# Performance work log

Hardware: AMD Instinct MI355X
Metric: run time of the kernel (lower is better)

## Reference

```python
import jax, jax.numpy as jnp
import numpy as np

EPS = 1e-5
G = 8    # groups
K = 3    # kernel_size


def bn(x, gamma, beta, mean, var):
    # inference-mode BatchNorm2d; x: (b,C,H,W), params: (C,)
    inv = gamma / jnp.sqrt(var + EPS)
    return x * inv[None, :, None, None] + (beta - mean * inv)[None, :, None, None]


def gconv1x1(x, w):
    # grouped 1x1 conv; x: (b, g*ci, H, W), w: (g, co, ci) -> (b, g*co, H, W)
    b, C, H, W = x.shape
    g, co, ci = w.shape
    xg = x.reshape(b, g, ci, H, W)
    y = jnp.einsum('bgihw,goi->bgohw', xg, w)
    return y.reshape(b, g * co, H, W)


def unfold3(x):
    # torch.nn.Unfold(k=3, stride=1, dilation=1, padding=1), reshaped to (b, C, 9, H, W)
    b, C, H, W = x.shape
    xp = jnp.pad(x, ((0, 0), (0, 0), (1, 1), (1, 1)))
    patches = [xp[:, :, i:i + H, j:j + W] for i in range(K) for j in range(K)]
    return jnp.stack(patches, axis=2)


def setup_inputs() -> dict:
    key = jax.random.key(0)
    ks = jax.random.split(key, 16)
    f = jax.random.normal
    u = jax.random.uniform
    return {
        'x':  f(ks[0], (2, 256, 128, 128), jnp.float32),
        'w1': f(ks[1], (8, 8, 32), jnp.float32) * 0.1,
        'b1': f(ks[2], (64,), jnp.float32) * 0.1,
        'g1': u(ks[3], (64,), jnp.float32, 0.5, 1.5),
        'be1': f(ks[4], (64,), jnp.float32) * 0.1,
        'm1': f(ks[5], (64,), jnp.float32) * 0.1,
        'v1': u(ks[6], (64,), jnp.float32, 0.5, 1.5),
        'w2': f(ks[7], (8, 10, 8), jnp.float32) * 0.1,
        'b2': f(ks[8], (80,), jnp.float32) * 0.1,
        'g2': u(ks[9], (80,), jnp.float32, 0.5, 1.5),
        'be2': f(ks[10], (80,), jnp.float32) * 0.1,
        'm2': f(ks[11], (80,), jnp.float32) * 0.1,
        'v2': u(ks[12], (80,), jnp.float32, 0.5, 1.5),
        'wv': f(ks[13], (8, 32, 32), jnp.float32) * 0.1,
    }


def reference(x, w1, b1, g1, be1, m1, v1, w2, b2, g2, be2, m2, v2, wv):
    b, C, H, W = x.shape
    # mask_conv: grouped 1x1 conv -> BN -> tanh -> grouped 1x1 conv -> BN
    t = jnp.tanh(bn(gconv1x1(x, w1) + b1[None, :, None, None], g1, be1, m1, v1))
    mn = bn(gconv1x1(t, w2) + b2[None, :, None, None], g2, be2, m2, v2)  # (b, G*(1+K*K), H, W)
    neighbor = mn[:, :G]          # (b, G, H, W)
    mask = mn[:, G:]              # (b, G*K*K, H, W)
    nb = unfold3(neighbor)        # (b, G, 9, H, W)
    logits = mask.reshape(b, G, K * K, H, W) + nb
    attn = jax.nn.softmax(logits, axis=2)               # (b, G, 9, H, W)
    # value path: grouped 1x1 conv (no bias) then unfold
    v = gconv1x1(x, wv)                                  # (b, C, H, W)
    vu = unfold3(v).reshape(b, G, C // G, K * K, H, W)   # (b, G, C/G, 9, H, W)
    out = jnp.einsum('bgkhw,bgckhw->bgchw', attn, vu)    # weighted sum over window
    return out.reshape(b, C, H, W)
```

## Files before the change

### kernel.cpp

```cpp
#include <hip/hip_runtime.h>

#define HW  16384
#define WD  128

#define TS   16
#define HS   18
#define HP   (HS * HS)
#define PRS  20
#define PLS  360
#define SROW 80

typedef __attribute__((ext_vector_type(8))) short bf16x8;
typedef __attribute__((ext_vector_type(4))) float f32x4;

__device__ __forceinline__ unsigned short f2bf(float f) {
    unsigned int u = __builtin_bit_cast(unsigned int, f);
    u += 0x7FFFu + ((u >> 16) & 1u);
    return (unsigned short)(u >> 16);
}
__device__ __forceinline__ float bf2f(unsigned int s) {
    return __builtin_bit_cast(float, (s & 0xFFFFu) << 16);
}
__device__ __forceinline__ float ftanh(float v) {
    const float e = __expf(2.0f * v);
    return 1.0f - __fdividef(2.0f, e + 1.0f);
}

__global__ __launch_bounds__(256) void la_t(
    const float* __restrict__ x,
    const float* __restrict__ w1, const float* __restrict__ b1,
    const float* __restrict__ g1, const float* __restrict__ be1,
    const float* __restrict__ m1, const float* __restrict__ v1,
    ushort4* __restrict__ t4, uint4* __restrict__ xbf)
{
    const int z   = blockIdx.x;
    const int b   = blockIdx.y;
    const int pix = blockIdx.z * blockDim.x + threadIdx.x;
    const int p   = z & 7;
    const int h   = z >> 3;

    const float* xp = x + (size_t)(b * 256 + p * 32) * HW + pix;
    float xv[32];
#pragma unroll
    for (int c = 0; c < 32; ++c) xv[c] = xp[(size_t)c * HW];

#pragma unroll
    for (int j = 0; j < 2; ++j) {
        const int c8 = h * 2 + j;
        uint4 u;
        u.x = (unsigned)f2bf(xv[c8 * 8 + 0]) | ((unsigned)f2bf(xv[c8 * 8 + 1]) << 16);
        u.y = (unsigned)f2bf(xv[c8 * 8 + 2]) | ((unsigned)f2bf(xv[c8 * 8 + 3]) << 16);
        u.z = (unsigned)f2bf(xv[c8 * 8 + 4]) | ((unsigned)f2bf(xv[c8 * 8 + 5]) << 16);
        u.w = (unsigned)f2bf(xv[c8 * 8 + 6]) | ((unsigned)f2bf(xv[c8 * 8 + 7]) << 16);
        xbf[((size_t)((b * 8 + p) * 4 + c8)) * HW + pix] = u;
    }

    const float* w1g = w1 + p * 256 + h * 4 * 32;
    float tv[4];
#pragma unroll
    for (int o = 0; o < 4; ++o) {
        float a = 0.f;
#pragma unroll
        for (int ci = 0; ci < 32; ++ci) a = fmaf(xv[ci], w1g[o * 32 + ci], a);
        const int ch = p * 8 + h * 4 + o;
        const float inv = g1[ch] * rsqrtf(v1[ch] + 1e-5f);
        const float add = be1[ch] + (b1[ch] - m1[ch]) * inv;
        tv[o] = ftanh(fmaf(a, inv, add));
    }

    t4[((size_t)((b * 8 + p) * 2 + h)) * HW + pix] =
        make_ushort4(f2bf(tv[0]), f2bf(tv[1]), f2bf(tv[2]), f2bf(tv[3]));
}

__global__ __launch_bounds__(256) void la_fused(
    const float* __restrict__ w2, const float* __restrict__ b2,
    const float* __restrict__ g2, const float* __restrict__ be2,
    const float* __restrict__ m2, const float* __restrict__ v2,
    const float* __restrict__ wv,
    const ushort4* __restrict__ t4, const uint4* __restrict__ xbf,
    float* __restrict__ out)
{
    __shared__ uint4 xt[4 * PLS];
    __shared__ float nbs[PLS];

    const int tid  = threadIdx.x;
    const int bg   = blockIdx.x;
    const int tile = blockIdx.y;
    const int b    = bg >> 3, g = bg & 7;
    const int ty0  = (tile >> 3) * TS;
    const int tx0  = (tile & 7) * TS;
    const int lane = tid & 63, wv4 = tid >> 6;

    const uint4*   xg = xbf + (size_t)((b * 8 + g) * 4) * HW;
    const ushort4* t0 = t4  + (size_t)(b * 16) * HW;

    const float* wvg = wv + g * 1024;
    bf16x8 bfrag[2];
#pragma unroll
    for (int nt = 0; nt < 2; ++nt) {
        const float* wp = wvg + (nt * 16 + (lane & 15)) * 32 + (lane >> 4) * 8;
        bf16x8 f;
#pragma unroll
        for (int j = 0; j < 8; ++j) f[j] = (short)f2bf(wp[j]);
        bfrag[nt] = f;
    }

    const int cy  = tid >> 4, cx = tid & 15;
    const int cpx = (ty0 + cy) * WD + (tx0 + cx);

    const int mc0    = 8 + 9 * g;
    const int pa     = mc0 / 10;
    const int pb     = (mc0 + 8) / 10;
    const int ksplit = 10 - (mc0 - pa * 10);

    const ushort4 tAlo = t4[((size_t)((b * 8 + pa) * 2 + 0)) * HW + cpx];
    const ushort4 tAhi = t4[((size_t)((b * 8 + pa) * 2 + 1)) * HW + cpx];
    const ushort4 tBlo = t4[((size_t)((b * 8 + pb) * 2 + 0)) * HW + cpx];
    const ushort4 tBhi = t4[((size_t)((b * 8 + pb) * 2 + 1)) * HW + cpx];

    const float inv2n = g2[g] * rsqrtf(v2[g] + 1e-5f);
    const float add2n = be2[g] + (b2[g] - m2[g]) * inv2n;

    for (int hp = tid; hp < HP; hp += 256) {
        const int hy = hp / HS, hx = hp - hy * HS;
        const int iy = ty0 + hy - 1, ix = tx0 + hx - 1;
        const int slot = hy * PRS + hx;
        if (((unsigned)iy < 128u) && ((unsigned)ix < 128u)) {
            const int po = iy * WD + ix;
            const ushort4 ta = t0[po];
            const ushort4 tb = t0[(size_t)HW + po];
            float an = 0.f;
            an = fmaf(bf2f(ta.x), w2[g * 8 + 0], an);
            an = fmaf(bf2f(ta.y), w2[g * 8 + 1], an);
            an = fmaf(bf2f(ta.z), w2[g * 8 + 2], an);
            an = fmaf(bf2f(ta.w), w2[g * 8 + 3], an);
            an = fmaf(bf2f(tb.x), w2[g * 8 + 4], an);
            an = fmaf(bf2f(tb.y), w2[g * 8 + 5], an);
            an = fmaf(bf2f(tb.z), w2[g * 8 + 6], an);
            an = fmaf(bf2f(tb.w), w2[g * 8 + 7], an);
            nbs[slot] = fmaf(an, inv2n, add2n);
#pragma unroll
            for (int c8 = 0; c8 < 4; ++c8)
                xt[c8 * PLS + slot] = xg[(size_t)c8 * HW + po];
        } else {
            const uint4 z = make_uint4(0u, 0u, 0u, 0u);
#pragma unroll
            for (int c8 = 0; c8 < 4; ++c8) xt[c8 * PLS + slot] = z;
            nbs[slot] = 0.f;
        }
    }
    __syncthreads();

    float tA[8], tB[8];
    tA[0] = bf2f(tAlo.x); tA[1] = bf2f(tAlo.y);
    tA[2] = bf2f(tAlo.z); tA[3] = bf2f(tAlo.w);
    tA[4] = bf2f(tAhi.x); tA[5] = bf2f(tAhi.y);
    tA[6] = bf2f(tAhi.z); tA[7] = bf2f(tAhi.w);
    tB[0] = bf2f(tBlo.x); tB[1] = bf2f(tBlo.y);
    tB[2] = bf2f(tBlo.z); tB[3] = bf2f(tBlo.w);
    tB[4] = bf2f(tBhi.x); tB[5] = bf2f(tBhi.y);
    tB[6] = bf2f(tBhi.z); tB[7] = bf2f(tBhi.w);

    float lg[9];
    float mx = -1e30f;
#pragma unroll
    for (int k = 0; k < 9; ++k) {
        const int mc = mc0 + k;
        const int p  = (k < ksplit) ? pa : pb;
        const int o  = mc - p * 10;
        const float* w2p = w2 + p * 80 + o * 8;
        float a = 0.f;
#pragma unroll
        for (int i = 0; i < 8; ++i) {
            const float ti = (k < ksplit) ? tA[i] : tB[i];
            a = fmaf(ti, w2p[i], a);
        }
        const float inv = g2[mc] * rsqrtf(v2[mc] + 1e-5f);
        const float add = be2[mc] + (b2[mc] - m2[mc]) * inv;
        lg[k] = fmaf(a, inv, add) + nbs[(cy + k / 3) * PRS + (cx + k % 3)];
        mx = fmaxf(mx, lg[k]);
    }
    float ssum = 0.f;
#pragma unroll
    for (int k = 0; k < 9; ++k) { lg[k] = __expf(lg[k] - mx); ssum += lg[k]; }
    const float rs = 1.f / ssum;

    float s[32];
#pragma unroll
    for (int c = 0; c < 32; ++c) s[c] = 0.f;
#pragma unroll
    for (int k = 0; k < 9; ++k) {
        const int slot = (cy + k / 3) * PRS + (cx + k % 3);
        const float e = lg[k];
#pragma unroll
        for (int c8 = 0; c8 < 4; ++c8) {
            const uint4 u = xt[c8 * PLS + slot];
            s[c8 * 8 + 0] = fmaf(e, bf2f(u.x),       s[c8 * 8 + 0]);
            s[c8 * 8 + 1] = fmaf(e, bf2f(u.x >> 16), s[c8 * 8 + 1]);
            s[c8 * 8 + 2] = fmaf(e, bf2f(u.y),       s[c8 * 8 + 2]);
            s[c8 * 8 + 3] = fmaf(e, bf2f(u.y >> 16), s[c8 * 8 + 3]);
            s[c8 * 8 + 4] = fmaf(e, bf2f(u.z),       s[c8 * 8 + 4]);
            s[c8 * 8 + 5] = fmaf(e, bf2f(u.z >> 16), s[c8 * 8 + 5]);
            s[c8 * 8 + 6] = fmaf(e, bf2f(u.w),       s[c8 * 8 + 6]);
            s[c8 * 8 + 7] = fmaf(e, bf2f(u.w >> 16), s[c8 * 8 + 7]);
        }
    }

    __syncthreads();
    char* Sb = (char*)xt;
    {
        uint4* row = (uint4*)(Sb + tid * SROW);
#pragma unroll
        for (int q = 0; q < 4; ++q) {
            uint4 u;
            u.x = (unsigned)f2bf(rs * s[q * 8 + 0]) | ((unsigned)f2bf(rs * s[q * 8 + 1]) << 16);
            u.y = (unsigned)f2bf(rs * s[q * 8 + 2]) | ((unsigned)f2bf(rs * s[q * 8 + 3]) << 16);
            u.z = (unsigned)f2bf(rs * s[q * 8 + 4]) | ((unsigned)f2bf(rs * s[q * 8 + 5]) << 16);
            u.w = (unsigned)f2bf(rs * s[q * 8 + 6]) | ((unsigned)f2bf(rs * s[q * 8 + 7]) << 16);
            row[q] = u;
        }
    }
    __syncthreads();

    float* outg = out + (size_t)(b * 256 + g * 32) * HW;
#pragma unroll
    for (int t = 0; t < 4; ++t) {
        const uint4 av = *(const uint4*)(Sb +
            (wv4 * 64 + t * 16 + (lane & 15)) * SROW + (lane >> 4) * 16);
        const bf16x8 af = __builtin_bit_cast(bf16x8, av);
#pragma unroll
        for (int nt = 0; nt < 2; ++nt) {
            f32x4 c = {0.f, 0.f, 0.f, 0.f};
            c = __builtin_amdgcn_mfma_f32_16x16x32_bf16(af, bfrag[nt], c, 0, 0, 0);
            const int ch  = nt * 16 + (lane & 15);
            const int idx = wv4 * 64 + t * 16 + 4 * (lane >> 4);
            const int oy  = ty0 + (idx >> 4), ox = tx0 + (idx & 15);
            f32x4* addr = (f32x4*)(outg + (size_t)ch * HW + oy * WD + ox);
            __builtin_nontemporal_store(c, addr);
        }
    }
}

extern "C" void kernel_launch(void* const* d_in, const int* in_sizes, int n_in,
                              void* d_out, int out_size, void* d_ws, size_t ws_size,
                              hipStream_t stream)
{
    const float* x   = (const float*)d_in[0];
    const float* w1  = (const float*)d_in[1];
    const float* b1  = (const float*)d_in[2];
    const float* g1  = (const float*)d_in[3];
    const float* be1 = (const float*)d_in[4];
    const float* m1  = (const float*)d_in[5];
    const float* v1  = (const float*)d_in[6];
    const float* w2  = (const float*)d_in[7];
    const float* b2  = (const float*)d_in[8];
    const float* g2  = (const float*)d_in[9];
    const float* be2 = (const float*)d_in[10];
    const float* m2  = (const float*)d_in[11];
    const float* v2  = (const float*)d_in[12];
    const float* wv  = (const float*)d_in[13];

    float* out = (float*)d_out;
    ushort4* t4  = (ushort4*)d_ws;
    uint4*   xbf = (uint4*)((char*)d_ws + (size_t)32 * HW * 8);

    dim3 blk(256);
    dim3 gt(16, 2, HW / 256);
    dim3 gfd(16, 64);

    hipLaunchKernelGGL(la_t, gt, blk, 0, stream,
                       x, w1, b1, g1, be1, m1, v1, t4, xbf);
    hipLaunchKernelGGL(la_fused, gfd, blk, 0, stream,
                       w2, b2, g2, be2, m2, v2, wv, t4, xbf, out);
}
```

Measured before the change: 124.3 us.

## Split value accumulation across two thread halves with 512-thread blocks

The fused attention kernel now launches 512 threads per block. Each half of the block accumulates 16 of the 32 value channels per pixel instead of one thread doing all 32, and each writes its half of the bf16 staging row. The MFMA output stage is spread over 8 waves with 2 row tiles each. This roughly halves the accumulator registers per thread and adds more waves to hide LDS and memory latency, at the cost of computing the softmax logits twice per pixel.

```diff
diff --git a/kernel.cpp b/kernel.cpp
--- a/kernel.cpp
+++ b/kernel.cpp
@@ -72,7 +72,7 @@
         make_ushort4(f2bf(tv[0]), f2bf(tv[1]), f2bf(tv[2]), f2bf(tv[3]));
 }
 
-__global__ __launch_bounds__(256) void la_fused(
+__global__ __launch_bounds__(512) void la_fused(
     const float* __restrict__ w2, const float* __restrict__ b2,
     const float* __restrict__ g2, const float* __restrict__ be2,
     const float* __restrict__ m2, const float* __restrict__ v2,
@@ -84,12 +84,14 @@
     __shared__ float nbs[PLS];
 
     const int tid  = threadIdx.x;
+    const int half = tid >> 8;
+    const int ptid = tid & 255;
     const int bg   = blockIdx.x;
     const int tile = blockIdx.y;
     const int b    = bg >> 3, g = bg & 7;
     const int ty0  = (tile >> 3) * TS;
     const int tx0  = (tile & 7) * TS;
-    const int lane = tid & 63, wv4 = tid >> 6;
+    const int lane = tid & 63, wave = tid >> 6;
 
     const uint4*   xg = xbf + (size_t)((b * 8 + g) * 4) * HW;
     const ushort4* t0 = t4  + (size_t)(b * 16) * HW;
@@ -105,7 +107,7 @@
         bfrag[nt] = f;
     }
 
-    const int cy  = tid >> 4, cx = tid & 15;
+    const int cy  = ptid >> 4, cx = ptid & 15;
     const int cpx = (ty0 + cy) * WD + (tx0 + cx);
 
     const int mc0    = 8 + 9 * g;
@@ -121,7 +123,7 @@
     const float inv2n = g2[g] * rsqrtf(v2[g] + 1e-5f);
     const float add2n = be2[g] + (b2[g] - m2[g]) * inv2n;
 
-    for (int hp = tid; hp < HP; hp += 256) {
+    for (int hp = tid; hp < HP; hp += 512) {
         const int hy = hp / HS, hx = hp - hy * HS;
         const int iy = ty0 + hy - 1, ix = tx0 + hx - 1;
         const int slot = hy * PRS + hx;
@@ -185,33 +187,33 @@
     for (int k = 0; k < 9; ++k) { lg[k] = __expf(lg[k] - mx); ssum += lg[k]; }
     const float rs = 1.f / ssum;
 
-    float s[32];
-#pragma unroll
-    for (int c = 0; c < 32; ++c) s[c] = 0.f;
+    float s[16];
+#pragma unroll
+    for (int c = 0; c < 16; ++c) s[c] = 0.f;
 #pragma unroll
     for (int k = 0; k < 9; ++k) {
         const int slot = (cy + k / 3) * PRS + (cx + k % 3);
         const float e = lg[k];
 #pragma unroll
-        for (int c8 = 0; c8 < 4; ++c8) {
-            const uint4 u = xt[c8 * PLS + slot];
-            s[c8 * 8 + 0] = fmaf(e, bf2f(u.x),       s[c8 * 8 + 0]);
-            s[c8 * 8 + 1] = fmaf(e, bf2f(u.x >> 16), s[c8 * 8 + 1]);
-            s[c8 * 8 + 2] = fmaf(e, bf2f(u.y),       s[c8 * 8 + 2]);
-            s[c8 * 8 + 3] = fmaf(e, bf2f(u.y >> 16), s[c8 * 8 + 3]);
-            s[c8 * 8 + 4] = fmaf(e, bf2f(u.z),       s[c8 * 8 + 4]);
-            s[c8 * 8 + 5] = fmaf(e, bf2f(u.z >> 16), s[c8 * 8 + 5]);
-            s[c8 * 8 + 6] = fmaf(e, bf2f(u.w),       s[c8 * 8 + 6]);
-            s[c8 * 8 + 7] = fmaf(e, bf2f(u.w >> 16), s[c8 * 8 + 7]);
+        for (int j = 0; j < 2; ++j) {
+            const uint4 u = xt[(half * 2 + j) * PLS + slot];
+            s[j * 8 + 0] = fmaf(e, bf2f(u.x),       s[j * 8 + 0]);
+            s[j * 8 + 1] = fmaf(e, bf2f(u.x >> 16), s[j * 8 + 1]);
+            s[j * 8 + 2] = fmaf(e, bf2f(u.y),       s[j * 8 + 2]);
+            s[j * 8 + 3] = fmaf(e, bf2f(u.y >> 16), s[j * 8 + 3]);
+            s[j * 8 + 4] = fmaf(e, bf2f(u.z),       s[j * 8 + 4]);
+            s[j * 8 + 5] = fmaf(e, bf2f(u.z >> 16), s[j * 8 + 5]);
+            s[j * 8 + 6] = fmaf(e, bf2f(u.w),       s[j * 8 + 6]);
+            s[j * 8 + 7] = fmaf(e, bf2f(u.w >> 16), s[j * 8 + 7]);
         }
     }
 
     __syncthreads();
     char* Sb = (char*)xt;
     {
-        uint4* row = (uint4*)(Sb + tid * SROW);
-#pragma unroll
-        for (int q = 0; q < 4; ++q) {
+        uint4* row = (uint4*)(Sb + ptid * SROW + half * 32);
+#pragma unroll
+        for (int q = 0; q < 2; ++q) {
             uint4 u;
             u.x = (unsigned)f2bf(rs * s[q * 8 + 0]) | ((unsigned)f2bf(rs * s[q * 8 + 1]) << 16);
             u.y = (unsigned)f2bf(rs * s[q * 8 + 2]) | ((unsigned)f2bf(rs * s[q * 8 + 3]) << 16);
@@ -224,17 +226,17 @@
 
     float* outg = out + (size_t)(b * 256 + g * 32) * HW;
 #pragma unroll
-    for (int t = 0; t < 4; ++t) {
+    for (int mt = 0; mt < 2; ++mt) {
+        const int m = wave * 2 + mt;
         const uint4 av = *(const uint4*)(Sb +
-            (wv4 * 64 + t * 16 + (lane & 15)) * SROW + (lane >> 4) * 16);
+            (m * 16 + (lane & 15)) * SROW + (lane >> 4) * 16);
         const bf16x8 af = __builtin_bit_cast(bf16x8, av);
 #pragma unroll
         for (int nt = 0; nt < 2; ++nt) {
             f32x4 c = {0.f, 0.f, 0.f, 0.f};
             c = __builtin_amdgcn_mfma_f32_16x16x32_bf16(af, bfrag[nt], c, 0, 0, 0);
-            const int ch  = nt * 16 + (lane & 15);
-            const int idx = wv4 * 64 + t * 16 + 4 * (lane >> 4);
-            const int oy  = ty0 + (idx >> 4), ox = tx0 + (idx & 15);
+            const int ch = nt * 16 + (lane & 15);
+            const int oy = ty0 + m, ox = tx0 + 4 * (lane >> 4);
             f32x4* addr = (f32x4*)(outg + (size_t)ch * HW + oy * WD + ox);
             __builtin_nontemporal_store(c, addr);
         }
@@ -264,12 +266,11 @@
     ushort4* t4  = (ushort4*)d_ws;
     uint4*   xbf = (uint4*)((char*)d_ws + (size_t)32 * HW * 8);
 
-    dim3 blk(256);
     dim3 gt(16, 2, HW / 256);
     dim3 gfd(16, 64);
 
-    hipLaunchKernelGGL(la_t, gt, blk, 0, stream,
+    hipLaunchKernelGGL(la_t, gt, dim3(256), 0, stream,
                        x, w1, b1, g1, be1, m1, v1, t4, xbf);
-    hipLaunchKernelGGL(la_fused, gfd, blk, 0, stream,
+    hipLaunchKernelGGL(la_fused, gfd, dim3(512), 0, stream,
                        w2, b2, g2, be2, m2, v2, wv, t4, xbf, out);
 }
```

New measurement: 128.1 us. 3.1% more time.
